# Kernel tuning notes

Hardware: AMD Instinct MI355X
Metric: run time of the kernel (lower is better)

The kernel has to match this reference:

```python
import jax, jax.numpy as jnp
import numpy as np

H = 1152      # embed_dim
NH = 16       # num heads
HD = H // NH  # head_dim = 72
SCALE = HD ** -0.5
B, S = 16, 729


def fake_quant(x, bits):
    """Symmetric per-tensor fake quantize-dequantize with straight-through estimator."""
    qmax = 2.0 ** (bits - 1) - 1.0
    scale = jnp.maximum(jnp.max(jnp.abs(x)), 1e-8) / qmax
    q = jnp.clip(jnp.round(x / scale), -qmax - 1.0, qmax) * scale
    return x + jax.lax.stop_gradient(q - x)  # STE


def fq_linear(x, W, b):
    # FakeQuantLinear: 8-bit fake-quant on activations and weights, fp accumulate
    return fake_quant(x, 8) @ fake_quant(W, 8).T + b


def setup_inputs() -> dict:
    key = jax.random.key(0)
    ks = jax.random.split(key, 9)
    std = H ** -0.5
    return {
        "hidden_states": jax.random.normal(ks[0], (B, S, H), jnp.float32),
        "Wq": jax.random.normal(ks[1], (H, H), jnp.float32) * std,
        "bq": jax.random.normal(ks[2], (H,), jnp.float32) * 0.02,
        "Wk": jax.random.normal(ks[3], (H, H), jnp.float32) * std,
        "bk": jax.random.normal(ks[4], (H,), jnp.float32) * 0.02,
        "Wv": jax.random.normal(ks[5], (H, H), jnp.float32) * std,
        "bv": jax.random.normal(ks[6], (H,), jnp.float32) * 0.02,
        "Wo": jax.random.normal(ks[7], (H, H), jnp.float32) * std,
        "bo": jax.random.normal(ks[8], (H,), jnp.float32) * 0.02,
    }


def reference(hidden_states, Wq, bq, Wk, bk, Wv, bv, Wo, bo):
    b, s, _ = hidden_states.shape
    q = fq_linear(hidden_states, Wq, bq).reshape(b, s, NH, HD).transpose(0, 2, 1, 3)
    k = fq_linear(hidden_states, Wk, bk).reshape(b, s, NH, HD).transpose(0, 2, 1, 3)
    v = fq_linear(hidden_states, Wv, bv).reshape(b, s, NH, HD).transpose(0, 2, 1, 3)
    # FakeQuantMatmul(8, 16): 8-bit quant on both matmul inputs, 16-bit quant on output
    attn = fake_quant(
        jnp.einsum("bhqd,bhkd->bhqk", fake_quant(q, 8), fake_quant(k, 8)), 16
    ) * SCALE
    # FakeQuantSoftmax(quant_bits=16): softmax then 16-bit fake quant
    attn = fake_quant(jax.nn.softmax(attn, axis=-1), 16)
    # FakeQuantMatmul(None, 8): no input quant, 8-bit output quant
    out = fake_quant(jnp.einsum("bhqk,bhkd->bhqd", attn, v), 8)
    out = out.transpose(0, 2, 1, 3).reshape(b, s, H)
    return fq_linear(out, Wo, bo)
```

## Files before the change

### kernel.cpp

```cpp
#include <hip/hip_runtime.h>
#include <math.h>

#define Hdim 1152
#define NHd  16
#define HDd  72
#define Bd   16
#define Sd   729
#define Ntok (Bd*Sd)
#define BHd  (Bd*NHd)
#define SCALE_F 0.117851130197757934f
#define LOG2E 1.44269504088896340736f

#define KFTB 8192
#define VFT 10240

#define SL_X 0
#define SL_WQ 1
#define SL_WK 2
#define SL_WV 3
#define SL_WO 4
#define SL_Q 5
#define SL_K 6
#define SL_LOGIT 8
#define SL_LMIN 9
#define SL_O 10

typedef short short8 __attribute__((ext_vector_type(8)));
typedef short short4v __attribute__((ext_vector_type(4)));
typedef float f32x4 __attribute__((ext_vector_type(4)));
typedef int int4v __attribute__((ext_vector_type(4)));

static __device__ __forceinline__ unsigned short f2bf(float f) {
  unsigned b = __float_as_uint(f);
  return (unsigned short)((b + 0x7FFFu + ((b >> 16) & 1u)) >> 16);
}
static __device__ __forceinline__ float bf2f(unsigned short u) {
  return __uint_as_float(((unsigned)u) << 16);
}
static __device__ __forceinline__ void atomicMaxF(float* p, float v) {
  atomicMax((unsigned int*)p, __float_as_uint(v));
}
static __device__ __forceinline__ void atomicMinF(float* p, float v) {
  atomicMin((unsigned int*)p, __float_as_uint(v));
}
static __device__ __forceinline__ float qscale(float mx, float qmax) {
  return fmaxf(mx, 1e-8f) / qmax;
}
static __device__ __forceinline__ float fexp2(float x) {
  float r; asm("v_exp_f32 %0, %1" : "=v"(r) : "v"(x)); return r;
}
static __device__ __forceinline__ float flog2(float x) {
  float r; asm("v_log_f32 %0, %1" : "=v"(r) : "v"(x)); return r;
}
static __device__ __forceinline__ short4v pack4(unsigned a, unsigned b, unsigned c, unsigned d) {
  union { unsigned u[2]; short4v s; } t;
  t.u[0] = a | (b << 16);
  t.u[1] = c | (d << 16);
  return t.s;
}
static __device__ __forceinline__ int q8i(float v, float s) {
  return (int)fminf(fmaxf(rintf(v / s), -128.f), 127.f);
}

#if __has_builtin(__builtin_amdgcn_mfma_f32_16x16x16bf16_1k)
#define MFMA16(a, b, c) __builtin_amdgcn_mfma_f32_16x16x16bf16_1k(a, b, c, 0, 0, 0)
#else
static __device__ __forceinline__ f32x4 MFMA16(short4v a, short4v b, f32x4 c) {
  asm("v_mfma_f32_16x16x16_bf16 %0, %1, %2, %0" : "+v"(c) : "v"(a), "v"(b));
  return c;
}
#endif
#if __has_builtin(__builtin_amdgcn_mfma_i32_16x16x64_i8)
#define MFMAI8(a, b, c) __builtin_amdgcn_mfma_i32_16x16x64_i8(a, b, c, 0, 0, 0)
#else
static __device__ __forceinline__ int4v MFMAI8(int4v a, int4v b, int4v c) {
  asm("v_mfma_i32_16x16x64_i8 %0, %1, %2, %0" : "+v"(c) : "v"(a), "v"(b));
  return c;
}
#endif

static __device__ __forceinline__ void gll16(const void* g, void* l) {
  __builtin_amdgcn_global_load_lds((const __attribute__((address_space(1))) void*)g,
                                   (__attribute__((address_space(3))) void*)l, 16, 0, 0);
}

__global__ void k_init(float* slots) {
  int i = threadIdx.x;
  if (i < 32) slots[i] = (i == SL_LMIN) ? __builtin_inff() : 0.0f;
}

__launch_bounds__(256)
__global__ void k_absmax(const float* __restrict__ X, const float* __restrict__ W0,
                         const float* __restrict__ W1, const float* __restrict__ W2,
                         const float* __restrict__ W3, float* slots) {
  int seg = blockIdx.y;
  const float* p; long n; int slot;
  if (seg == 0) { p = X; n = (long)Ntok * Hdim; slot = SL_X; }
  else {
    const float* ws4[4] = {W0, W1, W2, W3};
    p = ws4[seg - 1]; n = (long)Hdim * Hdim; slot = SL_WQ + seg - 1;
  }
  long n4 = n >> 2;
  const float4* p4 = (const float4*)p;
  float m = 0.f;
  for (long i = (long)blockIdx.x * blockDim.x + threadIdx.x; i < n4;
       i += (long)gridDim.x * blockDim.x) {
    float4 v = p4[i];
    m = fmaxf(m, fmaxf(fmaxf(fabsf(v.x), fabsf(v.y)), fmaxf(fabsf(v.z), fabsf(v.w))));
  }
  for (int off = 32; off; off >>= 1) m = fmaxf(m, __shfl_xor(m, off, 64));
  __shared__ float red[4];
  if ((threadIdx.x & 63) == 0) red[threadIdx.x >> 6] = m;
  __syncthreads();
  if (threadIdx.x == 0)
    atomicMaxF(&slots[slot], fmaxf(fmaxf(red[0], red[1]), fmaxf(red[2], red[3])));
}

__launch_bounds__(256)
__global__ void k_quant8i(const float* __restrict__ in, unsigned int* __restrict__ out,
                          long n, const float* __restrict__ slots, int slot) {
  float s = qscale(slots[slot], 127.0f);
  long n4 = n >> 2;
  const float4* in4 = (const float4*)in;
  for (long i = (long)blockIdx.x * blockDim.x + threadIdx.x; i < n4;
       i += (long)gridDim.x * blockDim.x) {
    float4 v = in4[i];
    unsigned a = (unsigned)q8i(v.x, s) & 255u;
    unsigned b = (unsigned)q8i(v.y, s) & 255u;
    unsigned c = (unsigned)q8i(v.z, s) & 255u;
    unsigned d = (unsigned)q8i(v.w, s) & 255u;
    out[i] = a | (b << 8) | (c << 16) | (d << 24);
  }
}

__launch_bounds__(256)
__global__ void k_quant8wi(const float* __restrict__ W0, const float* __restrict__ W1,
                           const float* __restrict__ W2, const float* __restrict__ W3,
                           unsigned int* O0, unsigned int* O1,
                           unsigned int* O2, unsigned int* O3,
                           const float* __restrict__ slots) {
  int seg = blockIdx.y;
  const float* ws4[4] = {W0, W1, W2, W3};
  unsigned int* os4[4] = {O0, O1, O2, O3};
  const float* in = ws4[seg];
  unsigned int* out = os4[seg];
  float s = qscale(slots[SL_WQ + seg], 127.0f);
  long n4 = ((long)Hdim * Hdim) >> 2;
  const float4* in4 = (const float4*)in;
  for (long i = (long)blockIdx.x * blockDim.x + threadIdx.x; i < n4;
       i += (long)gridDim.x * blockDim.x) {
    float4 v = in4[i];
    unsigned a = (unsigned)q8i(v.x, s) & 255u;
    unsigned b = (unsigned)q8i(v.y, s) & 255u;
    unsigned c = (unsigned)q8i(v.z, s) & 255u;
    unsigned d = (unsigned)q8i(v.w, s) & 255u;
    out[i] = a | (b << 8) | (c << 16) | (d << 24);
  }
}

#define GBM 128
#define GBN 128
static __device__ __forceinline__ void gemm_core(const char* __restrict__ A,
                                                 const char* __restrict__ Bm,
                                                 int bM, int bN, int tid,
                                                 char (*As)[GBM][64],
                                                 char (*Bs)[GBN][64],
                                                 int4v acc[4][4]) {
  int lane = tid & 63, wid = tid >> 6;
  int wm = wid >> 1, wn = wid & 1;
  int l15 = lane & 15, l4 = lane >> 4;
  int srow = lane >> 2;
  int scol = ((lane & 3) ^ ((lane >> 3) & 3)) * 16;
  const char* pa = A + ((long)(bM * GBM + wid * 32) + srow) * Hdim + scol;
  const char* pb = Bm + ((long)(bN * GBN + wid * 32) + srow) * Hdim + scol;
  int csw = (l4 ^ ((l15 >> 1) & 3)) * 16;

  for (int kt = 0; kt < 9; ++kt) {
    int kb = kt * 128;
    __syncthreads();
    gll16(pa + kb,                 &As[0][wid * 32][0]);
    gll16(pa + kb + 16 * Hdim,     &As[0][wid * 32 + 16][0]);
    gll16(pa + kb + 64,            &As[1][wid * 32][0]);
    gll16(pa + kb + 64 + 16 * Hdim,&As[1][wid * 32 + 16][0]);
    gll16(pb + kb,                 &Bs[0][wid * 32][0]);
    gll16(pb + kb + 16 * Hdim,     &Bs[0][wid * 32 + 16][0]);
    gll16(pb + kb + 64,            &Bs[1][wid * 32][0]);
    gll16(pb + kb + 64 + 16 * Hdim,&Bs[1][wid * 32 + 16][0]);
    __syncthreads();
#pragma unroll
    for (int t = 0; t < 2; ++t) {
      int4v af[4], bf4[4];
#pragma unroll
      for (int rf = 0; rf < 4; ++rf)
        af[rf] = *(const int4v*)&As[t][wm * 64 + rf * 16 + l15][csw];
#pragma unroll
      for (int cf = 0; cf < 4; ++cf)
        bf4[cf] = *(const int4v*)&Bs[t][wn * 64 + cf * 16 + l15][csw];
#pragma unroll
      for (int rf = 0; rf < 4; ++rf)
#pragma unroll
        for (int cf = 0; cf < 4; ++cf)
          acc[rf][cf] = MFMAI8(af[rf], bf4[cf], acc[rf][cf]);
    }
  }
}

__launch_bounds__(256, 3)
__global__ void k_gemm(const char* __restrict__ A,
                       const char* __restrict__ Bm,
                       const float* __restrict__ bias,
                       float* __restrict__ C,
                       float* slots, int slotA, int slotB, int slotOut) {
  __shared__ char As[2][GBM][64];
  __shared__ char Bs[2][GBN][64];
  __shared__ float red[4];
  int tid = threadIdx.x, lane = tid & 63, wid = tid >> 6;
  int wm = wid >> 1, wn = wid & 1;
  int l15 = lane & 15, l4 = lane >> 4;
  int bM = blockIdx.x, bN = blockIdx.y;
  int4v acc[4][4];
  for (int rf = 0; rf < 4; ++rf)
    for (int cf = 0; cf < 4; ++cf) acc[rf][cf] = int4v{0, 0, 0, 0};
  gemm_core(A, Bm, bM, bN, tid, As, Bs, acc);
  float alpha = qscale(slots[slotA], 127.f) * qscale(slots[slotB], 127.f);
  float lmax = 0.f;
#pragma unroll
  for (int cf = 0; cf < 4; ++cf) {
    int col = bN * GBN + wn * 64 + cf * 16 + l15;
    float bv = bias[col];
#pragma unroll
    for (int rf = 0; rf < 4; ++rf)
#pragma unroll
      for (int j = 0; j < 4; ++j) {
        int row = bM * GBM + wm * 64 + rf * 16 + l4 * 4 + j;
        if (row < Ntok) {
          float v = (float)acc[rf][cf][j] * alpha + bv;
          C[(long)row * Hdim + col] = v;
          lmax = fmaxf(lmax, fabsf(v));
        }
      }
  }
  if (slotOut >= 0) {
    for (int off = 32; off; off >>= 1) lmax = fmaxf(lmax, __shfl_xor(lmax, off, 64));
    if ((tid & 63) == 0) red[wid] = lmax;
    __syncthreads();
    if (tid == 0)
      atomicMaxF(&slots[slotOut], fmaxf(fmaxf(red[0], red[1]), fmaxf(red[2], red[3])));
  }
}

__launch_bounds__(256, 3)
__global__ void k_gemm3(const char* __restrict__ A,
                        const char* __restrict__ W0,
                        const char* __restrict__ W1,
                        const char* __restrict__ W2,
                        const float* __restrict__ b0, const float* __restrict__ b1,
                        const float* __restrict__ b2,
                        float* __restrict__ C0, float* __restrict__ C1,
                        float* __restrict__ C2, float* slots) {
  __shared__ char As[2][GBM][64];
  __shared__ char Bs[2][GBN][64];
  __shared__ float red[4];
  int bNg = blockIdx.y;
  int mi = bNg / 9, bN = bNg - mi * 9;
  const char* Bm = mi == 0 ? W0 : (mi == 1 ? W1 : W2);
  const float* bias = mi == 0 ? b0 : (mi == 1 ? b1 : b2);
  float* C = mi == 0 ? C0 : (mi == 1 ? C1 : C2);
  int slotB = SL_WQ + mi;
  int slotOut = mi == 0 ? SL_Q : (mi == 1 ? SL_K : -1);

  int tid = threadIdx.x, lane = tid & 63, wid = tid >> 6;
  int wm = wid >> 1, wn = wid & 1;
  int l15 = lane & 15, l4 = lane >> 4;
  int bM = blockIdx.x;
  int4v acc[4][4];
  for (int rf = 0; rf < 4; ++rf)
    for (int cf = 0; cf < 4; ++cf) acc[rf][cf] = int4v{0, 0, 0, 0};
  gemm_core(A, Bm, bM, bN, tid, As, Bs, acc);
  float alpha = qscale(slots[SL_X], 127.f) * qscale(slots[slotB], 127.f);
  float lmax = 0.f;
#pragma unroll
  for (int cf = 0; cf < 4; ++cf) {
    int col = bN * GBN + wn * 64 + cf * 16 + l15;
    float bv = bias[col];
#pragma unroll
    for (int rf = 0; rf < 4; ++rf)
#pragma unroll
      for (int j = 0; j < 4; ++j) {
        int row = bM * GBM + wm * 64 + rf * 16 + l4 * 4 + j;
        if (row < Ntok) {
          float v = (float)acc[rf][cf][j] * alpha + bv;
          C[(long)row * Hdim + col] = v;
          lmax = fmaxf(lmax, fabsf(v));
        }
      }
  }
  if (slotOut >= 0) {
    for (int off = 32; off; off >>= 1) lmax = fmaxf(lmax, __shfl_xor(lmax, off, 64));
    if ((tid & 63) == 0) red[wid] = lmax;
    __syncthreads();
    if (tid == 0)
      atomicMaxF(&slots[slotOut], fmaxf(fmaxf(red[0], red[1]), fmaxf(red[2], red[3])));
  }
}

__launch_bounds__(256)
__global__ void k_kfrag(const float* __restrict__ Kf, char* __restrict__ KF,
                        const float* __restrict__ slots) {
  int kt = blockIdx.x, bh = blockIdx.y;
  int b = bh >> 4, h = bh & 15;
  float s = qscale(slots[SL_K], 127.0f);
  int tid = threadIdx.x, lane = tid & 63, w = tid >> 6;
  int l15 = lane & 15, l4 = lane >> 4;
  long obase = ((long)(bh * 12 + kt)) * KFTB;
#pragma unroll
  for (int i = 0; i < 2; ++i) {
    int p = w * 2 + i;
    int cf = p >> 1, c = p & 1;
    int token = kt * 64 + cf * 16 + l15;
    char ov[16];
#pragma unroll
    for (int j = 0; j < 16; ++j) ov[j] = 0;
    if (token < Sd) {
      const float* src = &Kf[((long)(b * Sd + token)) * Hdim + h * HDd];
      if (c == 0) {
#pragma unroll
        for (int j = 0; j < 16; ++j) ov[j] = (char)q8i(src[l4 * 16 + j], s);
      } else if (l4 == 0) {
#pragma unroll
        for (int j = 0; j < 8; ++j) ov[j] = (char)q8i(src[64 + j], s);
      }
    }
    *(int4v*)&KF[obase + p * 1024 + lane * 16] = *(int4v*)ov;
  }
}

__launch_bounds__(256)
__global__ void k_vsplit(const float* __restrict__ Vf, unsigned short* __restrict__ VF) {
  int kt = blockIdx.x, bh = blockIdx.y;
  int b = bh >> 4, h = bh & 15;
  int tid = threadIdx.x, lane = tid & 63, w = tid >> 6;
  int l15 = lane & 15, l4 = lane >> 4;
  long obase = ((long)(bh * 12 + kt)) * VFT;
#pragma unroll
  for (int i = 0; i < 5; ++i) {
    int p = w + 4 * i;
    int dt = p >> 2, cf = p & 3;
    int d = dt * 16 + l15;
    int tok0 = kt * 64 + cf * 16 + l4 * 4;
    unsigned short u[8];
#pragma unroll
    for (int j = 0; j < 4; ++j) {
      int tok = tok0 + j;
      float v = 0.f;
      if (tok < Sd && d < HDd)
        v = Vf[((long)(b * Sd + tok)) * Hdim + h * HDd + d];
      unsigned short hb = f2bf(v);
      u[j] = hb;
      u[4 + j] = f2bf(v - bf2f(hb));
    }
    *(short8*)&VF[obase + (long)p * 512 + lane * 8] = *(short8*)u;
  }
}

static __device__ __forceinline__ void loadQ8(const char* __restrict__ Qq,
                                              int b, int h, int qc, int l4,
                                              int4v& qa, int4v& qb) {
  const char* qp = &Qq[((long)(b * Sd + qc)) * Hdim + h * HDd];
  union { long l[2]; int4v v; } u0, u1;
  u0.l[0] = *(const long*)(qp + l4 * 16);
  u0.l[1] = *(const long*)(qp + l4 * 16 + 8);
  qa = u0.v;
  u1.l[0] = (l4 == 0) ? *(const long*)(qp + 64) : 0L;
  u1.l[1] = 0L;
  qb = u1.v;
}

__launch_bounds__(256, 4)
__global__ void k_attnA(const char* __restrict__ Qq,
                        const char* __restrict__ KF, float* slots) {
  __shared__ float red[4];
  int qh = blockIdx.x, bh = blockIdx.y;
  int b = bh >> 4, h = bh & 15;
  int tid = threadIdx.x, lane = tid & 63, w = tid >> 6;
  int l15 = lane & 15, l4 = lane >> 4;
  const char* kfb = KF + (long)bh * 12 * KFTB;
  int4v qa[3], qb[3];
#pragma unroll
  for (int qs = 0; qs < 3; ++qs) {
    int qrow = (qh * 3 + qs) * 64 + w * 16 + l15;
    int qc = qrow > Sd - 1 ? Sd - 1 : qrow;
    loadQ8(Qq, b, h, qc, l4, qa[qs], qb[qs]);
  }
  float mx = 0.f;
#pragma unroll 1
  for (int kt = 0; kt < 12; ++kt) {
    int4v kf[8];
#pragma unroll
    for (int p = 0; p < 8; ++p)
      kf[p] = *(const int4v*)&kfb[(long)kt * KFTB + p * 1024 + lane * 16];
#pragma unroll
    for (int qs = 0; qs < 3; ++qs) {
#pragma unroll
      for (int cf = 0; cf < 4; ++cf) {
        int4v a = int4v{0, 0, 0, 0};
        a = MFMAI8(kf[cf * 2 + 0], qa[qs], a);
        a = MFMAI8(kf[cf * 2 + 1], qb[qs], a);
#pragma unroll
        for (int j = 0; j < 4; ++j) mx = fmaxf(mx, fabsf((float)a[j]));
      }
    }
  }
  mx *= qscale(slots[SL_Q], 127.f) * qscale(slots[SL_K], 127.f);
  for (int off = 32; off; off >>= 1) mx = fmaxf(mx, __shfl_xor(mx, off, 64));
  if ((tid & 63) == 0) red[w] = mx;
  __syncthreads();
  if (tid == 0)
    atomicMaxF(&slots[SL_LOGIT], fmaxf(fmaxf(red[0], red[1]), fmaxf(red[2], red[3])));
}

__launch_bounds__(256, 4)
__global__ void k_attnB(const char* __restrict__ Qq,
                        const char* __restrict__ KF, float* slots,
                        float* __restrict__ m_arr, float* __restrict__ l_arr) {
  __shared__ float red[4];
  int qh = blockIdx.x, bh = blockIdx.y;
  int b = bh >> 4, h = bh & 15;
  int tid = threadIdx.x, lane = tid & 63, w = tid >> 6;
  int l15 = lane & 15, l4 = lane >> 4;
  const char* kfb = KF + (long)bh * 12 * KFTB;
  int4v qa[3], qb[3];
#pragma unroll
  for (int qs = 0; qs < 3; ++qs) {
    int qrow = (qh * 3 + qs) * 64 + w * 16 + l15;
    int qc = qrow > Sd - 1 ? Sd - 1 : qrow;
    loadQ8(Qq, b, h, qc, l4, qa[qs], qb[qs]);
  }
  float s16 = qscale(slots[SL_LOGIT], 32767.f);
  float sqk = qscale(slots[SL_Q], 127.f) * qscale(slots[SL_K], 127.f);
  float c0 = sqk / s16;
  float c1e = s16 * SCALE_F * LOG2E;
  float m_run[3] = {-3.0e38f, -3.0e38f, -3.0e38f};
  float l_run[3] = {0.f, 0.f, 0.f};
#pragma unroll 1
  for (int kt = 0; kt < 12; ++kt) {
    int4v kf[8];
#pragma unroll
    for (int p = 0; p < 8; ++p)
      kf[p] = *(const int4v*)&kfb[(long)kt * KFTB + p * 1024 + lane * 16];
#pragma unroll
    for (int qs = 0; qs < 3; ++qs) {
      float nv[16];
#pragma unroll
      for (int cf = 0; cf < 4; ++cf) {
        int4v a = int4v{0, 0, 0, 0};
        a = MFMAI8(kf[cf * 2 + 0], qa[qs], a);
        a = MFMAI8(kf[cf * 2 + 1], qb[qs], a);
#pragma unroll
        for (int j = 0; j < 4; ++j) nv[cf * 4 + j] = rintf((float)a[j] * c0);
      }
      if (kt == 11) {
#pragma unroll
        for (int cf = 0; cf < 4; ++cf)
#pragma unroll
          for (int j = 0; j < 4; ++j) {
            int kcol = 704 + cf * 16 + l4 * 4 + j;
            if (kcol > Sd - 1) nv[cf * 4 + j] = -3.0e30f;
          }
      }
      float mt = nv[0];
#pragma unroll
      for (int i = 1; i < 16; ++i) mt = fmaxf(mt, nv[i]);
      mt = fmaxf(mt, __shfl_xor(mt, 16, 64));
      mt = fmaxf(mt, __shfl_xor(mt, 32, 64));
      float mn = fmaxf(m_run[qs], mt);
      float f = fexp2((m_run[qs] - mn) * c1e);
      float se = 0.f;
#pragma unroll
      for (int i = 0; i < 16; ++i) se += fexp2((nv[i] - mn) * c1e);
      se += __shfl_xor(se, 16, 64);
      se += __shfl_xor(se, 32, 64);
      l_run[qs] = l_run[qs] * f + se;
      m_run[qs] = mn;
    }
  }
  float lmin = 3.0e38f;
#pragma unroll
  for (int qs = 0; qs < 3; ++qs) {
    int qrow = (qh * 3 + qs) * 64 + w * 16 + l15;
    if (qrow < Sd) {
      if (l4 == 0) {
        m_arr[bh * Sd + qrow] = m_run[qs];
        l_arr[bh * Sd + qrow] = l_run[qs];
      }
      lmin = fminf(lmin, l_run[qs]);
    }
  }
  for (int off = 32; off; off >>= 1) lmin = fminf(lmin, __shfl_xor(lmin, off, 64));
  if ((tid & 63) == 0) red[w] = lmin;
  __syncthreads();
  if (tid == 0)
    atomicMinF(&slots[SL_LMIN], fminf(fminf(red[0], red[1]), fminf(red[2], red[3])));
}

__launch_bounds__(256, 5)
__global__ void k_attnC(const char* __restrict__ Qq,
                        const char* __restrict__ KF,
                        const unsigned short* __restrict__ VF,
                        const float* __restrict__ m_arr, const float* __restrict__ l_arr,
                        float* slots, float* __restrict__ O) {
  __shared__ char Ks[KFTB];
  __shared__ unsigned short Vs[VFT];
  __shared__ float red[4];
  int qp, bh;
  {
    int id = blockIdx.y * 6 + blockIdx.x;
    int xcd = id & 7, sub = id >> 3;
    int bhl = sub / 6;
    qp = sub - bhl * 6;
    bh = xcd * 32 + bhl;
  }
  int b = bh >> 4, h = bh & 15;
  int tid = threadIdx.x, lane = tid & 63, w = tid >> 6;
  int l15 = lane & 15, l4 = lane >> 4;
  float s16 = qscale(slots[SL_LOGIT], 32767.f);
  float sqk = qscale(slots[SL_Q], 127.f) * qscale(slots[SL_K], 127.f);
  float c0 = sqk / s16;
  float c1e = s16 * SCALE_F * LOG2E;
  float pmaxv = 1.0f / slots[SL_LMIN];
  float sp = fmaxf(pmaxv, 1e-8f) / 32767.0f;
  float inv_sp = 1.0f / sp;
  int4v qa[2], qb[2];
  float dexp[2];
#pragma unroll
  for (int qs = 0; qs < 2; ++qs) {
    int qrow = (qp * 2 + qs) * 64 + w * 16 + l15;
    int qc = qrow > Sd - 1 ? Sd - 1 : qrow;
    loadQ8(Qq, b, h, qc, l4, qa[qs], qb[qs]);
    float mn = m_arr[bh * Sd + qc];
    float c2 = (1.0f / l_arr[bh * Sd + qc]) * inv_sp;
    dexp[qs] = flog2(c2) - mn * c1e;
  }
  const char* kfb = KF + (long)bh * 12 * KFTB;
  const unsigned short* vfb = VF + (long)bh * 12 * VFT;
  f32x4 acc[2][5];
#pragma unroll
  for (int qs = 0; qs < 2; ++qs)
#pragma unroll
    for (int i = 0; i < 5; ++i) acc[qs][i] = f32x4{0.f, 0.f, 0.f, 0.f};

#pragma unroll 1
  for (int kt = 0; kt < 12; ++kt) {
    __syncthreads();
    {
      const char* kg = kfb + (long)kt * KFTB;
#pragma unroll
      for (int i = 0; i < 2; ++i) {
        int c = w * 2 + i;
        gll16(kg + c * 1024 + lane * 16, &Ks[c * 1024]);
      }
      const unsigned short* vg = vfb + (long)kt * VFT;
#pragma unroll
      for (int i = 0; i < 5; ++i) {
        int c = w + 4 * i;
        gll16(vg + c * 512 + lane * 8, &Vs[c * 512]);
      }
    }
    __syncthreads();
#pragma unroll
    for (int cf = 0; cf < 4; ++cf) {
      int4v k0 = *(const int4v*)&Ks[(cf * 2 + 0) * 1024 + lane * 16];
      int4v k1 = *(const int4v*)&Ks[(cf * 2 + 1) * 1024 + lane * 16];
      short4v Pp[2], Pr[2];
#pragma unroll
      for (int qs = 0; qs < 2; ++qs) {
        int4v a = int4v{0, 0, 0, 0};
        a = MFMAI8(k0, qa[qs], a);
        a = MFMAI8(k1, qb[qs], a);
        unsigned phb[4], rsb[4];
#pragma unroll
        for (int j = 0; j < 4; ++j) {
          float n = rintf((float)a[j] * c0);
          float nn = rintf(fexp2(fmaf(n, c1e, dexp[qs])));
          unsigned ub = __float_as_uint(nn);
          unsigned hb = ub & 0xFFFF0000u;
          float rsf = nn - __uint_as_float(hb);
          phb[j] = hb >> 16;
          rsb[j] = __float_as_uint(rsf) >> 16;
        }
        Pp[qs] = pack4(phb[0], phb[1], phb[2], phb[3]);
        Pr[qs] = pack4(rsb[0], rsb[1], rsb[2], rsb[3]);
      }
#pragma unroll
      for (int dt = 0; dt < 5; ++dt) {
        short8 vv = *(const short8*)&Vs[(dt * 4 + cf) * 512 + lane * 8];
        short4v vh = __builtin_shufflevector(vv, vv, 0, 1, 2, 3);
        short4v vl = __builtin_shufflevector(vv, vv, 4, 5, 6, 7);
#pragma unroll
        for (int qs = 0; qs < 2; ++qs) {
          acc[qs][dt] = MFMA16(Pp[qs], vh, acc[qs][dt]);
          acc[qs][dt] = MFMA16(Pp[qs], vl, acc[qs][dt]);
          acc[qs][dt] = MFMA16(Pr[qs], vh, acc[qs][dt]);
        }
      }
    }
  }
  float lmax = 0.f;
#pragma unroll
  for (int qs = 0; qs < 2; ++qs)
#pragma unroll
    for (int dt = 0; dt < 5; ++dt) {
      int d = dt * 16 + l15;
#pragma unroll
      for (int j = 0; j < 4; ++j) {
        int qr = (qp * 2 + qs) * 64 + w * 16 + l4 * 4 + j;
        if (qr < Sd && d < HDd) {
          float v = sp * acc[qs][dt][j];
          O[((long)(b * Sd + qr)) * Hdim + h * HDd + d] = v;
          lmax = fmaxf(lmax, fabsf(v));
        }
      }
    }
  for (int off = 32; off; off >>= 1) lmax = fmaxf(lmax, __shfl_xor(lmax, off, 64));
  if ((tid & 63) == 0) red[w] = lmax;
  __syncthreads();
  if (tid == 0)
    atomicMaxF(&slots[SL_O], fmaxf(fmaxf(red[0], red[1]), fmaxf(red[2], red[3])));
}

extern "C" void kernel_launch(void* const* d_in, const int* in_sizes, int n_in,
                              void* d_out, int out_size, void* d_ws, size_t ws_size,
                              hipStream_t stream) {
  const float* Xin = (const float*)d_in[0];
  const float* Wq = (const float*)d_in[1];
  const float* bq = (const float*)d_in[2];
  const float* Wk = (const float*)d_in[3];
  const float* bk = (const float*)d_in[4];
  const float* Wv = (const float*)d_in[5];
  const float* bv = (const float*)d_in[6];
  const float* Wo = (const float*)d_in[7];
  const float* bo = (const float*)d_in[8];
  float* out = (float*)d_out;
  char* ws = (char*)d_ws;

  size_t off = 0;
  auto alloc = [&](size_t bytes) {
    void* p = ws + off;
    off = (off + bytes + 255) & ~(size_t)255;
    return p;
  };
  float* slots = (float*)alloc(256);
  char* Xq  = (char*)alloc((size_t)Ntok * Hdim);
  char* Wqq = (char*)alloc((size_t)Hdim * Hdim);
  char* Wkq = (char*)alloc((size_t)Hdim * Hdim);
  char* Wvq = (char*)alloc((size_t)Hdim * Hdim);
  char* Woq = (char*)alloc((size_t)Hdim * Hdim);
  float* Kf = (float*)alloc((size_t)Ntok * Hdim * 4);
  float* Vf = (float*)alloc((size_t)Ntok * Hdim * 4);
  char* Qq = (char*)alloc((size_t)Ntok * Hdim);
  char* KFr = (char*)alloc((size_t)BHd * 12 * KFTB);
  unsigned short* VFr = (unsigned short*)alloc((size_t)BHd * 12 * VFT * 2);
  float* m_arr = (float*)alloc((size_t)BHd * Sd * 4);
  float* l_arr = (float*)alloc((size_t)BHd * Sd * 4);
  char* Oq = (char*)Vf;
  float* Qf = out;
  float* Of = out;

  k_init<<<1, 64, 0, stream>>>(slots);
  k_absmax<<<dim3(256, 5), 256, 0, stream>>>(Xin, Wq, Wk, Wv, Wo, slots);
  k_quant8i<<<1024, 256, 0, stream>>>(Xin, (unsigned int*)Xq, (long)Ntok * Hdim, slots, SL_X);
  k_quant8wi<<<dim3(128, 4), 256, 0, stream>>>(Wq, Wk, Wv, Wo, (unsigned int*)Wqq,
                                               (unsigned int*)Wkq, (unsigned int*)Wvq,
                                               (unsigned int*)Woq, slots);

  k_gemm3<<<dim3(92, 27), 256, 0, stream>>>(Xq, Wqq, Wkq, Wvq, bq, bk, bv,
                                            Qf, Kf, Vf, slots);

  k_quant8i<<<1024, 256, 0, stream>>>(Qf, (unsigned int*)Qq, (long)Ntok * Hdim, slots, SL_Q);
  k_kfrag<<<dim3(12, 256), 256, 0, stream>>>(Kf, KFr, slots);
  k_vsplit<<<dim3(12, 256), 256, 0, stream>>>(Vf, VFr);

  k_attnA<<<dim3(4, 256), 256, 0, stream>>>(Qq, KFr, slots);
  k_attnB<<<dim3(4, 256), 256, 0, stream>>>(Qq, KFr, slots, m_arr, l_arr);
  k_attnC<<<dim3(6, 256), 256, 0, stream>>>(Qq, KFr, VFr, m_arr, l_arr, slots, Of);

  k_quant8i<<<1024, 256, 0, stream>>>(Of, (unsigned int*)Oq, (long)Ntok * Hdim, slots, SL_O);
  k_gemm<<<dim3(92, 9), 256, 0, stream>>>(Oq, Woq, bo, out, slots, SL_O, SL_WO, -1);
}
```

Baseline: 468.2 us.

## Double-buffer int8 GEMM K-loop and read attention K directly from global

The int8 GEMM core now uses a 64-wide K step across two LDS buffers, prefetching the next tile while the current one runs MFMAs, with manual vmcnt waits and barriers. Occupancy hints for both GEMM kernels rise from 3 to 4 blocks. In the attention PV kernel, K fragments are read straight from global memory instead of through LDS, and QK/softmax work for later chunks is interleaved with PV MFMAs so V loading overlaps compute. The goal is to hide load latency and cut LDS traffic, at the cost of more register pressure and uncached, uncoalesced-risk global reads for K.

```diff
diff --git a/kernel.cpp b/kernel.cpp
--- a/kernel.cpp
+++ b/kernel.cpp
@@ -175,37 +175,42 @@
   const char* pb = Bm + ((long)(bN * GBN + wid * 32) + srow) * Hdim + scol;
   int csw = (l4 ^ ((l15 >> 1) & 3)) * 16;
 
-  for (int kt = 0; kt < 9; ++kt) {
-    int kb = kt * 128;
-    __syncthreads();
-    gll16(pa + kb,                 &As[0][wid * 32][0]);
-    gll16(pa + kb + 16 * Hdim,     &As[0][wid * 32 + 16][0]);
-    gll16(pa + kb + 64,            &As[1][wid * 32][0]);
-    gll16(pa + kb + 64 + 16 * Hdim,&As[1][wid * 32 + 16][0]);
-    gll16(pb + kb,                 &Bs[0][wid * 32][0]);
-    gll16(pb + kb + 16 * Hdim,     &Bs[0][wid * 32 + 16][0]);
-    gll16(pb + kb + 64,            &Bs[1][wid * 32][0]);
-    gll16(pb + kb + 64 + 16 * Hdim,&Bs[1][wid * 32 + 16][0]);
-    __syncthreads();
-#pragma unroll
-    for (int t = 0; t < 2; ++t) {
-      int4v af[4], bf4[4];
-#pragma unroll
-      for (int rf = 0; rf < 4; ++rf)
-        af[rf] = *(const int4v*)&As[t][wm * 64 + rf * 16 + l15][csw];
+  auto stage = [&](int buf, int kt) {
+    int kb = kt * 64;
+    gll16(pa + kb, &As[buf][wid * 32][0]);
+    gll16(pa + kb + 16 * Hdim, &As[buf][wid * 32 + 16][0]);
+    gll16(pb + kb, &Bs[buf][wid * 32][0]);
+    gll16(pb + kb + 16 * Hdim, &Bs[buf][wid * 32 + 16][0]);
+  };
+
+  stage(0, 0);
+#pragma unroll 1
+  for (int kt = 0; kt < 18; ++kt) {
+    int cur = kt & 1;
+    if (kt < 17) {
+      stage(cur ^ 1, kt + 1);
+      asm volatile("s_waitcnt vmcnt(4)" ::: "memory");
+    } else {
+      asm volatile("s_waitcnt vmcnt(0)" ::: "memory");
+    }
+    asm volatile("s_barrier" ::: "memory");
+    int4v af[4], bf4[4];
+#pragma unroll
+    for (int rf = 0; rf < 4; ++rf)
+      af[rf] = *(const int4v*)&As[cur][wm * 64 + rf * 16 + l15][csw];
+#pragma unroll
+    for (int cf = 0; cf < 4; ++cf)
+      bf4[cf] = *(const int4v*)&Bs[cur][wn * 64 + cf * 16 + l15][csw];
+#pragma unroll
+    for (int rf = 0; rf < 4; ++rf)
 #pragma unroll
       for (int cf = 0; cf < 4; ++cf)
-        bf4[cf] = *(const int4v*)&Bs[t][wn * 64 + cf * 16 + l15][csw];
-#pragma unroll
-      for (int rf = 0; rf < 4; ++rf)
-#pragma unroll
-        for (int cf = 0; cf < 4; ++cf)
-          acc[rf][cf] = MFMAI8(af[rf], bf4[cf], acc[rf][cf]);
-    }
-  }
-}
-
-__launch_bounds__(256, 3)
+        acc[rf][cf] = MFMAI8(af[rf], bf4[cf], acc[rf][cf]);
+    asm volatile("s_barrier" ::: "memory");
+  }
+}
+
+__launch_bounds__(256, 4)
 __global__ void k_gemm(const char* __restrict__ A,
                        const char* __restrict__ Bm,
                        const float* __restrict__ bias,
@@ -249,7 +254,7 @@
   }
 }
 
-__launch_bounds__(256, 3)
+__launch_bounds__(256, 4)
 __global__ void k_gemm3(const char* __restrict__ A,
                         const char* __restrict__ W0,
                         const char* __restrict__ W1,
@@ -509,7 +514,6 @@
                         const unsigned short* __restrict__ VF,
                         const float* __restrict__ m_arr, const float* __restrict__ l_arr,
                         float* slots, float* __restrict__ O) {
-  __shared__ char Ks[KFTB];
   __shared__ unsigned short Vs[VFT];
   __shared__ float red[4];
   int qp, bh;
@@ -553,12 +557,6 @@
   for (int kt = 0; kt < 12; ++kt) {
     __syncthreads();
     {
-      const char* kg = kfb + (long)kt * KFTB;
-#pragma unroll
-      for (int i = 0; i < 2; ++i) {
-        int c = w * 2 + i;
-        gll16(kg + c * 1024 + lane * 16, &Ks[c * 1024]);
-      }
       const unsigned short* vg = vfb + (long)kt * VFT;
 #pragma unroll
       for (int i = 0; i < 5; ++i) {
@@ -566,12 +564,13 @@
         gll16(vg + c * 512 + lane * 8, &Vs[c * 512]);
       }
     }
-    __syncthreads();
-#pragma unroll
-    for (int cf = 0; cf < 4; ++cf) {
-      int4v k0 = *(const int4v*)&Ks[(cf * 2 + 0) * 1024 + lane * 16];
-      int4v k1 = *(const int4v*)&Ks[(cf * 2 + 1) * 1024 + lane * 16];
-      short4v Pp[2], Pr[2];
+    const char* kg = kfb + (long)kt * KFTB;
+    short4v Pp[4], Pr[4];
+    short4v Pq[4];
+    short4v Rq[4];
+    auto computeP = [&](int cf) {
+      int4v k0 = *(const int4v*)&kg[(cf * 2 + 0) * 1024 + lane * 16];
+      int4v k1 = *(const int4v*)&kg[(cf * 2 + 1) * 1024 + lane * 16];
 #pragma unroll
       for (int qs = 0; qs < 2; ++qs) {
         int4v a = int4v{0, 0, 0, 0};
@@ -588,22 +587,36 @@
           phb[j] = hb >> 16;
           rsb[j] = __float_as_uint(rsf) >> 16;
         }
-        Pp[qs] = pack4(phb[0], phb[1], phb[2], phb[3]);
-        Pr[qs] = pack4(rsb[0], rsb[1], rsb[2], rsb[3]);
-      }
+        if (qs == 0) { Pp[cf] = pack4(phb[0], phb[1], phb[2], phb[3]);
+                       Pr[cf] = pack4(rsb[0], rsb[1], rsb[2], rsb[3]); }
+        else         { Pq[cf] = pack4(phb[0], phb[1], phb[2], phb[3]);
+                       Rq[cf] = pack4(rsb[0], rsb[1], rsb[2], rsb[3]); }
+      }
+    };
+    auto pv = [&](int cf) {
 #pragma unroll
       for (int dt = 0; dt < 5; ++dt) {
         short8 vv = *(const short8*)&Vs[(dt * 4 + cf) * 512 + lane * 8];
         short4v vh = __builtin_shufflevector(vv, vv, 0, 1, 2, 3);
         short4v vl = __builtin_shufflevector(vv, vv, 4, 5, 6, 7);
-#pragma unroll
-        for (int qs = 0; qs < 2; ++qs) {
-          acc[qs][dt] = MFMA16(Pp[qs], vh, acc[qs][dt]);
-          acc[qs][dt] = MFMA16(Pp[qs], vl, acc[qs][dt]);
-          acc[qs][dt] = MFMA16(Pr[qs], vh, acc[qs][dt]);
-        }
-      }
-    }
+        acc[0][dt] = MFMA16(Pp[cf], vh, acc[0][dt]);
+        acc[0][dt] = MFMA16(Pp[cf], vl, acc[0][dt]);
+        acc[0][dt] = MFMA16(Pr[cf], vh, acc[0][dt]);
+        acc[1][dt] = MFMA16(Pq[cf], vh, acc[1][dt]);
+        acc[1][dt] = MFMA16(Pq[cf], vl, acc[1][dt]);
+        acc[1][dt] = MFMA16(Rq[cf], vh, acc[1][dt]);
+      }
+    };
+    computeP(0);
+    computeP(1);
+    asm volatile("s_waitcnt vmcnt(0)" ::: "memory");
+    asm volatile("s_barrier" ::: "memory");
+    pv(0);
+    computeP(2);
+    pv(1);
+    computeP(3);
+    pv(2);
+    pv(3);
   }
   float lmax = 0.f;
 #pragma unroll
```

Measured after the change: 564.3 us. +20.5%, slower.

## Double-buffer int8 GEMM k-loop with async global-to-LDS prefetch

Applied to the files above, without the earlier changes.

The int8 MFMA GEMM core now runs 18 steps of 64-wide k, each prefetching the next slice into the alternate LDS buffer before computing on the current one. Explicit vmcnt waits and raw s_barrier replace the two __syncthreads per iteration, so global loads overlap the MFMA work. Launch bounds are raised from 3 to 4 blocks per CU for both GEMM kernels, which tightens register limits. The risk is that hand-written waitcnt and barrier placement depends on exact load counts, and lower register budgets may cause spills.

```diff
diff --git a/kernel.cpp b/kernel.cpp
--- a/kernel.cpp
+++ b/kernel.cpp
@@ -175,37 +175,42 @@
   const char* pb = Bm + ((long)(bN * GBN + wid * 32) + srow) * Hdim + scol;
   int csw = (l4 ^ ((l15 >> 1) & 3)) * 16;
 
-  for (int kt = 0; kt < 9; ++kt) {
-    int kb = kt * 128;
-    __syncthreads();
-    gll16(pa + kb,                 &As[0][wid * 32][0]);
-    gll16(pa + kb + 16 * Hdim,     &As[0][wid * 32 + 16][0]);
-    gll16(pa + kb + 64,            &As[1][wid * 32][0]);
-    gll16(pa + kb + 64 + 16 * Hdim,&As[1][wid * 32 + 16][0]);
-    gll16(pb + kb,                 &Bs[0][wid * 32][0]);
-    gll16(pb + kb + 16 * Hdim,     &Bs[0][wid * 32 + 16][0]);
-    gll16(pb + kb + 64,            &Bs[1][wid * 32][0]);
-    gll16(pb + kb + 64 + 16 * Hdim,&Bs[1][wid * 32 + 16][0]);
-    __syncthreads();
-#pragma unroll
-    for (int t = 0; t < 2; ++t) {
-      int4v af[4], bf4[4];
-#pragma unroll
-      for (int rf = 0; rf < 4; ++rf)
-        af[rf] = *(const int4v*)&As[t][wm * 64 + rf * 16 + l15][csw];
+  auto stage = [&](int buf, int kt) {
+    int kb = kt * 64;
+    gll16(pa + kb, &As[buf][wid * 32][0]);
+    gll16(pa + kb + 16 * Hdim, &As[buf][wid * 32 + 16][0]);
+    gll16(pb + kb, &Bs[buf][wid * 32][0]);
+    gll16(pb + kb + 16 * Hdim, &Bs[buf][wid * 32 + 16][0]);
+  };
+
+  stage(0, 0);
+#pragma unroll 1
+  for (int kt = 0; kt < 18; ++kt) {
+    int cur = kt & 1;
+    if (kt < 17) {
+      stage(cur ^ 1, kt + 1);
+      asm volatile("s_waitcnt vmcnt(4)" ::: "memory");
+    } else {
+      asm volatile("s_waitcnt vmcnt(0)" ::: "memory");
+    }
+    asm volatile("s_barrier" ::: "memory");
+    int4v af[4], bf4[4];
+#pragma unroll
+    for (int rf = 0; rf < 4; ++rf)
+      af[rf] = *(const int4v*)&As[cur][wm * 64 + rf * 16 + l15][csw];
+#pragma unroll
+    for (int cf = 0; cf < 4; ++cf)
+      bf4[cf] = *(const int4v*)&Bs[cur][wn * 64 + cf * 16 + l15][csw];
+#pragma unroll
+    for (int rf = 0; rf < 4; ++rf)
 #pragma unroll
       for (int cf = 0; cf < 4; ++cf)
-        bf4[cf] = *(const int4v*)&Bs[t][wn * 64 + cf * 16 + l15][csw];
-#pragma unroll
-      for (int rf = 0; rf < 4; ++rf)
-#pragma unroll
-        for (int cf = 0; cf < 4; ++cf)
-          acc[rf][cf] = MFMAI8(af[rf], bf4[cf], acc[rf][cf]);
-    }
-  }
-}
-
-__launch_bounds__(256, 3)
+        acc[rf][cf] = MFMAI8(af[rf], bf4[cf], acc[rf][cf]);
+    asm volatile("s_barrier" ::: "memory");
+  }
+}
+
+__launch_bounds__(256, 4)
 __global__ void k_gemm(const char* __restrict__ A,
                        const char* __restrict__ Bm,
                        const float* __restrict__ bias,
@@ -249,7 +254,7 @@
   }
 }
 
-__launch_bounds__(256, 3)
+__launch_bounds__(256, 4)
 __global__ void k_gemm3(const char* __restrict__ A,
                         const char* __restrict__ W0,
                         const char* __restrict__ W1,
```

Result: faster. 450.2 us (-3.8%).
